# Optimization experiments

Hardware: AMD Instinct MI355X
Metric: run time of the kernel (lower is better)

The kernel has to match this reference:

```python
import jax, jax.numpy as jnp
import numpy as np

N = 20000      # nodes
E = 640000     # edges
FIN = 128
FQK = 128
FV = 128
H = 8
FH = FQK // H   # 16
FHV = FV // H   # 16
FTOT = 2 * FQK + FV


def setup_inputs() -> dict:
    key = jax.random.key(0)
    kx, kw, ks, kd, kb = jax.random.split(key, 5)
    x = jax.random.normal(kx, (N, FIN), dtype=jnp.float32)
    # nn.Linear(Fin, Ftot, bias=False): weight [Ftot, Fin]
    W = jax.random.normal(kw, (FTOT, FIN), dtype=jnp.float32) / np.sqrt(FIN)
    # src must be sorted (scatter ops assume grouped-by-src, size src[-1]+1)
    src = jnp.sort(jax.random.randint(ks, (E,), 0, N, dtype=jnp.int64))
    src = src.at[-1].set(N - 1)  # ensure full output size N
    dest = jax.random.randint(kd, (E,), 0, N, dtype=jnp.int64)
    ei = jnp.stack([src, dest])
    batch = jnp.sort(jax.random.randint(kb, (N,), 0, 16, dtype=jnp.int64))
    return {"x": x, "W": W, "batch": batch, "ei": ei}


def reference(x, W, batch, ei):
    src, dest = ei[0], ei[1]
    scaling = float(FH) ** (-0.5)
    proj = x @ W.T                                  # [N, Ftot]
    q, k, v = jnp.split(proj, [FQK, 2 * FQK], axis=-1)
    q = (q * scaling).reshape(-1, H, FH)            # [N, H, Fh]
    k = k.reshape(-1, H, FH)
    v = v.reshape(-1, H, FHV)
    qs, ks, vs = q[src], k[dest], v[dest]           # [E, H, Fh] gathers
    aw = jnp.einsum('ehf,ehf->eh', qs, ks)          # per-edge dot products
    # scatter_softmax: global (not per-segment) max subtraction, as in source
    xm = aw.max(axis=0)                              # [H]
    exp = jnp.exp(aw - xm) + 1e-8                    # [E, H]
    expsum = jax.ops.segment_sum(exp, src, num_segments=N)[src]
    attn = exp / expsum                              # [E, H]
    out = jax.ops.segment_sum(attn[:, :, None] * vs, src, num_segments=N)
    return out.reshape(-1, H * FHV)                  # [N, Fv]
```

## Files before the change

### kernel.cpp

```cpp
#include <hip/hip_runtime.h>

constexpr int FIN = 128;

constexpr float XM0 = 8.0f;

typedef __attribute__((ext_vector_type(8))) short bf8x;
typedef __attribute__((ext_vector_type(4))) float f4x;
typedef _Float16 h2 __attribute__((ext_vector_type(2)));

__device__ inline unsigned short f2bf(float v) {
  unsigned int u = __float_as_uint(v);
  unsigned int r = u + 0x7FFFu + ((u >> 16) & 1u);
  return (unsigned short)(r >> 16);
}
__device__ inline float bf2f(unsigned short s) {
  return __uint_as_float(((unsigned int)s) << 16);
}
__device__ inline unsigned short f2h(float v) {
  _Float16 h = (_Float16)v;
  return __builtin_bit_cast(unsigned short, h);
}
__device__ inline h2 bch2(float f) { return __builtin_bit_cast(h2, f); }
__device__ inline float bcf(h2 h) { return __builtin_bit_cast(float, h); }

__device__ inline float dot2acc(h2 a, h2 b, float c) {
#if __has_builtin(__builtin_amdgcn_fdot2)
  return __builtin_amdgcn_fdot2(a, b, c, false);
#else
  return c + (float)a[0] * (float)b[0] + (float)a[1] * (float)b[1];
#endif
}

__global__ __launch_bounds__(256, 2) void proj_kernel(
    const float* __restrict__ x, const float* __restrict__ W,
    unsigned short* __restrict__ qn, unsigned short* __restrict__ kvn, int N,
    const int* __restrict__ src, const int* __restrict__ dest,
    unsigned short* __restrict__ dest16, int* __restrict__ row_ptr, int E) {
  __shared__ unsigned short xhi[128][72], xlo[128][72];
  __shared__ unsigned short whi[128][72], wlo[128][72];

  const int tid = threadIdx.x;
  const int r0 = blockIdx.y * 128;
  const int c0 = blockIdx.x * 128;

  {
    const int gid = (blockIdx.y * gridDim.x + blockIdx.x) * 256 + tid;
    const int tot = gridDim.x * gridDim.y * 256;
    for (int i = gid; i < E; i += tot) dest16[i] = (unsigned short)dest[i];
    if (gid <= N) {
      int lo = 0, hi = E;
      while (lo < hi) {
        int mid = (lo + hi) >> 1;
        if (src[mid] < gid) lo = mid + 1; else hi = mid;
      }
      row_ptr[gid] = lo;
    }
  }

  const int lane = tid & 63;
  const int w = tid >> 6;
  const int mbase = (w >> 1) * 64;
  const int nbase = (w & 1) * 64;
  const int lr = lane & 15;
  const int q4 = lane >> 4;

  f4x acc[4][4];
#pragma unroll
  for (int mt = 0; mt < 4; ++mt)
#pragma unroll
    for (int nt = 0; nt < 4; ++nt)
#pragma unroll
      for (int k = 0; k < 4; ++k) acc[mt][nt][k] = 0.f;

  for (int p = 0; p < 2; ++p) {
    if (p) __syncthreads();
#pragma unroll
    for (int pass = 0; pass < 8; ++pass) {
      const int idx = tid + pass * 256;
      const int kq = idx & 15, r = idx >> 4;
      float4 xv = make_float4(0.f, 0.f, 0.f, 0.f);
      if (r0 + r < N) xv = *(const float4*)(x + (size_t)(r0 + r) * FIN + p * 64 + kq * 4);
      const float4 wv = *(const float4*)(W + (size_t)(c0 + r) * FIN + p * 64 + kq * 4);
      const float xa[4] = {xv.x, xv.y, xv.z, xv.w};
      const float wa[4] = {wv.x, wv.y, wv.z, wv.w};
      unsigned short xh[4], xl[4], wh[4], wl[4];
#pragma unroll
      for (int i = 0; i < 4; ++i) {
        xh[i] = f2bf(xa[i]); xl[i] = f2bf(xa[i] - bf2f(xh[i]));
        wh[i] = f2bf(wa[i]); wl[i] = f2bf(wa[i] - bf2f(wh[i]));
      }
      *(ushort4*)&xhi[r][kq * 4] = make_ushort4(xh[0], xh[1], xh[2], xh[3]);
      *(ushort4*)&xlo[r][kq * 4] = make_ushort4(xl[0], xl[1], xl[2], xl[3]);
      *(ushort4*)&whi[r][kq * 4] = make_ushort4(wh[0], wh[1], wh[2], wh[3]);
      *(ushort4*)&wlo[r][kq * 4] = make_ushort4(wl[0], wl[1], wl[2], wl[3]);
    }
    __syncthreads();

#pragma unroll
    for (int kit = 0; kit < 2; ++kit) {
      const int ko = kit * 32 + q4 * 8;
      bf8x ah[4], al[4], bh[4], bl[4];
#pragma unroll
      for (int i2 = 0; i2 < 4; ++i2) {
        ah[i2] = *(const bf8x*)&xhi[mbase + i2 * 16 + lr][ko];
        al[i2] = *(const bf8x*)&xlo[mbase + i2 * 16 + lr][ko];
        bh[i2] = *(const bf8x*)&whi[nbase + i2 * 16 + lr][ko];
        bl[i2] = *(const bf8x*)&wlo[nbase + i2 * 16 + lr][ko];
      }
#pragma unroll
      for (int mt = 0; mt < 4; ++mt)
#pragma unroll
        for (int nt = 0; nt < 4; ++nt) {
          acc[mt][nt] = __builtin_amdgcn_mfma_f32_16x16x32_bf16(ah[mt], bh[nt], acc[mt][nt], 0, 0, 0);
          acc[mt][nt] = __builtin_amdgcn_mfma_f32_16x16x32_bf16(ah[mt], bl[nt], acc[mt][nt], 0, 0, 0);
          acc[mt][nt] = __builtin_amdgcn_mfma_f32_16x16x32_bf16(al[mt], bh[nt], acc[mt][nt], 0, 0, 0);
        }
    }
  }

#pragma unroll
  for (int mt = 0; mt < 4; ++mt)
#pragma unroll
    for (int nt = 0; nt < 4; ++nt)
#pragma unroll
      for (int rr = 0; rr < 4; ++rr) {
        const int row = r0 + mbase + mt * 16 + q4 * 4 + rr;
        if (row < N) {
          const int c = c0 + nbase + nt * 16 + lr;
          const float v = acc[mt][nt][rr];
          if (c < 128) {
            qn[(size_t)row * 128 + c] = f2h(v * 0.25f);
          } else if (c < 256) {
            kvn[(size_t)row * 256 + (c - 128)] = f2h(v);
          } else {
            kvn[(size_t)row * 256 + 128 + (c - 256)] = f2h(v);
          }
        }
      }
}

__global__ __launch_bounds__(256, 8) void attn_kernel(
    const unsigned short* __restrict__ qn_, const unsigned short* __restrict__ kvn_,
    const unsigned short* __restrict__ dest16, const int* __restrict__ row_ptr,
    float* __restrict__ out, int N) {
  const _Float16* qn = (const _Float16*)qn_;
  const _Float16* kvn = (const _Float16*)kvn_;

  const int lane = threadIdx.x & 63;
  const int wid = __builtin_amdgcn_readfirstlane(threadIdx.x >> 6);
  const int n = blockIdx.x * 4 + wid;
  if (n >= N) return;

  const int e_grp = lane >> 4;
  const int seg = lane & 15;

  const int e0 = row_ptr[n], e1 = row_ptr[n + 1];

  h2 q2[4];
  {
    const float4 qv = *(const float4*)(qn + (size_t)n * 128 + seg * 8);
    q2[0] = bch2(qv.x); q2[1] = bch2(qv.y); q2[2] = bch2(qv.z); q2[3] = bch2(qv.w);
  }

  h2 acc4[4] = {h2{0, 0}, h2{0, 0}, h2{0, 0}, h2{0, 0}};
  float es = 0.f;

  for (int cb = e0; cb < e1; cb += 64) {
    const int ee = cb + lane;
    const int dv = dest16[(ee < e1) ? ee : (e1 - 1)];

    const int rem = e1 - cb;
    const int nch = (rem < 64) ? ((rem + 3) >> 2) : 16;

    auto ldkv = [&](int j, float4& kk, float4& vv) {
      const int sl = j * 4 + e_grp;
      const int d = __shfl(dv, sl);
      const _Float16* kp = kvn + (size_t)d * 256 + seg * 8;
      kk = *(const float4*)kp;
      vv = *(const float4*)(kp + 128);
    };

    auto comp = [&](int j, const float4& kk, const float4& vv) {
      float p = 0.f;
      p = dot2acc(q2[0], bch2(kk.x), p);
      p = dot2acc(q2[1], bch2(kk.y), p);
      p = dot2acc(q2[2], bch2(kk.z), p);
      p = dot2acc(q2[3], bch2(kk.w), p);
      const float s = p + __shfl_xor(p, 1);
      const int e = cb + j * 4 + e_grp;
      const float a = (e < e1) ? (__expf(s - XM0) + 1e-8f) : 0.f;
      es += a;
      const _Float16 a1 = (_Float16)a;
      const h2 av = {a1, a1};
      acc4[0] = __builtin_elementwise_fma(av, bch2(vv.x), acc4[0]);
      acc4[1] = __builtin_elementwise_fma(av, bch2(vv.y), acc4[1]);
      acc4[2] = __builtin_elementwise_fma(av, bch2(vv.z), acc4[2]);
      acc4[3] = __builtin_elementwise_fma(av, bch2(vv.w), acc4[3]);
    };

    float4 kkA, vvA, kkB, vvB;
    ldkv(0, kkA, vvA);
    ldkv(1, kkB, vvB);

    for (int j = 0; j < nch; j += 2) {
      float4 kkA2, vvA2, kkB2, vvB2;
      const bool pf = (j + 2 < nch);
      if (pf) { ldkv(j + 2, kkA2, vvA2); ldkv(j + 3, kkB2, vvB2); }
      comp(j, kkA, vvA);
      comp(j + 1, kkB, vvB);
      if (pf) { kkA = kkA2; vvA = vvA2; kkB = kkB2; vvB = vvB2; }
    }
  }

#pragma unroll
  for (int st = 16; st <= 32; st <<= 1) {
#pragma unroll
    for (int j = 0; j < 4; ++j) {
      const h2 o = bch2(__shfl_xor(bcf(acc4[j]), st));
      acc4[j] = acc4[j] + o;
    }
    es += __shfl_xor(es, st);
  }

  if (e_grp == 0) {
    const float inv = (e1 > e0) ? (1.0f / es) : 0.f;
    float o[8];
#pragma unroll
    for (int j = 0; j < 4; ++j) {
      o[2 * j] = (float)acc4[j][0] * inv;
      o[2 * j + 1] = (float)acc4[j][1] * inv;
    }
    float* op = out + (size_t)n * 128 + seg * 8;
    *(float4*)op = make_float4(o[0], o[1], o[2], o[3]);
    *(float4*)(op + 4) = make_float4(o[4], o[5], o[6], o[7]);
  }
}

extern "C" void kernel_launch(void* const* d_in, const int* in_sizes, int n_in,
                              void* d_out, int out_size, void* d_ws, size_t ws_size,
                              hipStream_t stream) {
  const float* x = (const float*)d_in[0];
  const float* W = (const float*)d_in[1];
  const int* ei = (const int*)d_in[3];

  const int N = in_sizes[0] / FIN;
  const int E = in_sizes[3] / 2;
  const int* src = ei;
  const int* dst = ei + E;
  float* out = (float*)d_out;

  char* ws = (char*)d_ws;
  unsigned short* qn = (unsigned short*)ws;
  size_t off = (size_t)N * 128 * sizeof(unsigned short);
  unsigned short* kvn = (unsigned short*)(ws + off);
  off += (size_t)N * 256 * sizeof(unsigned short);
  unsigned short* dest16 = (unsigned short*)(ws + off);
  off += ((size_t)E * sizeof(unsigned short) + 15) & ~15ull;
  int* row_ptr = (int*)(ws + off);

  dim3 pgrid(3, (N + 127) / 128);
  proj_kernel<<<pgrid, 256, 0, stream>>>(x, W, qn, kvn, N, src, dst, dest16, row_ptr, E);
  attn_kernel<<<(N + 3) / 4, 256, 0, stream>>>(qn, kvn, dest16, row_ptr, out, N);
}
```

Measured before the change: 124.7 us.

## Split heads into two groups with separate K/V planes per group

Q, K and V are now stored in two head-group planes, each holding 4 heads per node. The attention kernel launches twice as many blocks, and each wave handles one head group for one node with 8 edges in flight per chunk instead of 4. Each gathered row shrinks from 512 B to 256 B per group, so the K/V working set per plane is halved, which is meant to improve L2 locality and parallelism. In exchange, edge indices and row_ptr are read twice and the projection stores are more scattered.

```diff
diff --git a/kernel.cpp b/kernel.cpp
--- a/kernel.cpp
+++ b/kernel.cpp
@@ -33,7 +33,7 @@
 
 __global__ __launch_bounds__(256, 2) void proj_kernel(
     const float* __restrict__ x, const float* __restrict__ W,
-    unsigned short* __restrict__ qn, unsigned short* __restrict__ kvn, int N,
+    unsigned short* __restrict__ qg, unsigned short* __restrict__ kvg, int N,
     const int* __restrict__ src, const int* __restrict__ dest,
     unsigned short* __restrict__ dest16, int* __restrict__ row_ptr, int E) {
   __shared__ unsigned short xhi[128][72], xlo[128][72];
@@ -129,39 +129,49 @@
           const int c = c0 + nbase + nt * 16 + lr;
           const float v = acc[mt][nt][rr];
           if (c < 128) {
-            qn[(size_t)row * 128 + c] = f2h(v * 0.25f);
+            const int head = c >> 4, g = head >> 2, hg = head & 3;
+            const int seg = hg * 2 + ((c >> 3) & 1), feat = c & 7;
+            qg[((size_t)g * N + row) * 64 + seg * 8 + feat] = f2h(v * 0.25f);
           } else if (c < 256) {
-            kvn[(size_t)row * 256 + (c - 128)] = f2h(v);
+            const int cc = c - 128;
+            const int head = cc >> 4, g = head >> 2, hg = head & 3;
+            const int seg = hg * 2 + ((cc >> 3) & 1), feat = cc & 7;
+            kvg[((size_t)g * N + row) * 128 + seg * 8 + feat] = f2h(v);
           } else {
-            kvn[(size_t)row * 256 + 128 + (c - 256)] = f2h(v);
+            const int cc = c - 256;
+            const int head = cc >> 4, g = head >> 2, hg = head & 3;
+            const int seg = hg * 2 + ((cc >> 3) & 1), feat = cc & 7;
+            kvg[((size_t)g * N + row) * 128 + 64 + seg * 8 + feat] = f2h(v);
           }
         }
       }
 }
 
 __global__ __launch_bounds__(256, 8) void attn_kernel(
-    const unsigned short* __restrict__ qn_, const unsigned short* __restrict__ kvn_,
+    const unsigned short* __restrict__ qg_, const unsigned short* __restrict__ kvg_,
     const unsigned short* __restrict__ dest16, const int* __restrict__ row_ptr,
     float* __restrict__ out, int N) {
-  const _Float16* qn = (const _Float16*)qn_;
-  const _Float16* kvn = (const _Float16*)kvn_;
+  const _Float16* qg = (const _Float16*)qg_;
+  const _Float16* kvg = (const _Float16*)kvg_;
 
   const int lane = threadIdx.x & 63;
   const int wid = __builtin_amdgcn_readfirstlane(threadIdx.x >> 6);
-  const int n = blockIdx.x * 4 + wid;
+  const int g = blockIdx.x & 1;
+  const int n = (blockIdx.x >> 1) * 4 + wid;
   if (n >= N) return;
 
-  const int e_grp = lane >> 4;
-  const int seg = lane & 15;
+  const int seg = lane & 7;
+  const int slot = lane >> 3;
 
   const int e0 = row_ptr[n], e1 = row_ptr[n + 1];
 
   h2 q2[4];
   {
-    const float4 qv = *(const float4*)(qn + (size_t)n * 128 + seg * 8);
+    const float4 qv = *(const float4*)(qg + ((size_t)g * N + n) * 64 + seg * 8);
     q2[0] = bch2(qv.x); q2[1] = bch2(qv.y); q2[2] = bch2(qv.z); q2[3] = bch2(qv.w);
   }
 
+  const _Float16* kvb = kvg + (size_t)g * N * 128;
   h2 acc4[4] = {h2{0, 0}, h2{0, 0}, h2{0, 0}, h2{0, 0}};
   float es = 0.f;
 
@@ -170,14 +180,14 @@
     const int dv = dest16[(ee < e1) ? ee : (e1 - 1)];
 
     const int rem = e1 - cb;
-    const int nch = (rem < 64) ? ((rem + 3) >> 2) : 16;
+    const int nch = (rem < 64) ? ((rem + 7) >> 3) : 8;
 
     auto ldkv = [&](int j, float4& kk, float4& vv) {
-      const int sl = j * 4 + e_grp;
+      const int sl = j * 8 + slot;
       const int d = __shfl(dv, sl);
-      const _Float16* kp = kvn + (size_t)d * 256 + seg * 8;
+      const _Float16* kp = kvb + (size_t)d * 128 + seg * 8;
       kk = *(const float4*)kp;
-      vv = *(const float4*)(kp + 128);
+      vv = *(const float4*)(kp + 64);
     };
 
     auto comp = [&](int j, const float4& kk, const float4& vv) {
@@ -187,7 +197,7 @@
       p = dot2acc(q2[2], bch2(kk.z), p);
       p = dot2acc(q2[3], bch2(kk.w), p);
       const float s = p + __shfl_xor(p, 1);
-      const int e = cb + j * 4 + e_grp;
+      const int e = cb + j * 8 + slot;
       const float a = (e < e1) ? (__expf(s - XM0) + 1e-8f) : 0.f;
       es += a;
       const _Float16 a1 = (_Float16)a;
@@ -213,7 +223,7 @@
   }
 
 #pragma unroll
-  for (int st = 16; st <= 32; st <<= 1) {
+  for (int st = 8; st <= 32; st <<= 1) {
 #pragma unroll
     for (int j = 0; j < 4; ++j) {
       const h2 o = bch2(__shfl_xor(bcf(acc4[j]), st));
@@ -222,15 +232,17 @@
     es += __shfl_xor(es, st);
   }
 
-  if (e_grp == 0) {
+  if (slot == 0) {
     const float inv = (e1 > e0) ? (1.0f / es) : 0.f;
+    const int head = g * 4 + (seg >> 1);
+    const int half = seg & 1;
     float o[8];
 #pragma unroll
     for (int j = 0; j < 4; ++j) {
       o[2 * j] = (float)acc4[j][0] * inv;
       o[2 * j + 1] = (float)acc4[j][1] * inv;
     }
-    float* op = out + (size_t)n * 128 + seg * 8;
+    float* op = out + (size_t)n * 128 + head * 16 + half * 8;
     *(float4*)op = make_float4(o[0], o[1], o[2], o[3]);
     *(float4*)(op + 4) = make_float4(o[4], o[5], o[6], o[7]);
   }
@@ -250,15 +262,15 @@
   float* out = (float*)d_out;
 
   char* ws = (char*)d_ws;
-  unsigned short* qn = (unsigned short*)ws;
-  size_t off = (size_t)N * 128 * sizeof(unsigned short);
-  unsigned short* kvn = (unsigned short*)(ws + off);
-  off += (size_t)N * 256 * sizeof(unsigned short);
+  unsigned short* qg = (unsigned short*)ws;
+  size_t off = (size_t)2 * N * 64 * sizeof(unsigned short);
+  unsigned short* kvg = (unsigned short*)(ws + off);
+  off += (size_t)2 * N * 128 * sizeof(unsigned short);
   unsigned short* dest16 = (unsigned short*)(ws + off);
   off += ((size_t)E * sizeof(unsigned short) + 15) & ~15ull;
   int* row_ptr = (int*)(ws + off);
 
   dim3 pgrid(3, (N + 127) / 128);
-  proj_kernel<<<pgrid, 256, 0, stream>>>(x, W, qn, kvn, N, src, dst, dest16, row_ptr, E);
-  attn_kernel<<<(N + 3) / 4, 256, 0, stream>>>(qn, kvn, dest16, row_ptr, out, N);
-}
+  proj_kernel<<<pgrid, 256, 0, stream>>>(x, W, qg, kvg, N, src, dst, dest16, row_ptr, E);
+  attn_kernel<<<((N + 3) / 4) * 2, 256, 0, stream>>>(qg, kvg, dest16, row_ptr, out, N);
+}
```

Result: faster. 115.7 us, median of 2 (-7.2%).
